# Kernel optimization log

Measured on AMD Instinct MI355X. Metric: run time of the kernel, lower is better.

## Reference

```python
import jax, jax.numpy as jnp
import numpy as np

BUCKET_SIZE = 64
N_HASHES = 8
SELF_ATTN_VALUE = -5e4  # TOKEN_SELF_ATTN_VALUE
EPS = 1e-12  # F.normalize eps


def setup_inputs() -> dict:
    key = jax.random.key(0)
    k1, k2, k3 = jax.random.split(key, 3)
    B, S, D = 16, 4096, 128
    n_buckets = S // BUCKET_SIZE  # 64
    qk = jax.random.normal(k1, (B, S, D), dtype=jnp.float32)
    v = jax.random.normal(k2, (B, S, D), dtype=jnp.float32)
    # rotations_shape = (1, dim, n_hashes, n_buckets // 2); shared across batch
    rotations = jax.random.normal(k3, (1, D, N_HASHES, n_buckets // 2), dtype=jnp.float32)
    return {"qk": qk, "v": v, "rotations": rotations}


def _hash_vectors(qk, rotations, n_buckets):
    # qk: (B,S,D), rotations: (1,D,H,n_buckets//2)
    rotated = jnp.einsum('btf,fhi->bhti', qk, rotations[0])  # (B,H,S,nb/2)
    rotated = jnp.concatenate([rotated, -rotated], axis=-1)   # (B,H,S,nb)
    buckets = jnp.argmax(rotated, axis=-1)                    # (B,H,S)
    offsets = (jnp.arange(N_HASHES) * n_buckets)[None, :, None]
    return (buckets + offsets).reshape(qk.shape[0], -1)       # (B, H*S)


def _look_one_back(x):
    # concat each chunk with its predecessor (circular), along the window dim
    return jnp.concatenate([x, jnp.roll(x, 1, axis=1)], axis=2)


def reference(qk, v, rotations):
    B, S, D = qk.shape
    H = N_HASHES
    n_buckets = S // BUCKET_SIZE
    buckets = _hash_vectors(qk, rotations, n_buckets)         # (B, H*S) int

    ticker = jnp.broadcast_to(jnp.arange(H * S)[None, :], (B, H * S))
    buckets_and_t = S * buckets + (ticker % S)                # unique keys
    sticker = jnp.argsort(buckets_and_t, axis=-1)             # sort by bucket
    undo_sort = jnp.argsort(sticker, axis=-1)

    st = sticker % S                                          # original positions
    sqk = jnp.take_along_axis(qk, st[..., None], axis=1)      # (B,H*S,D)
    sv = jnp.take_along_axis(v, st[..., None], axis=1)

    C = H * n_buckets                                         # num chunks
    bq_t = st.reshape(B, C, -1)                               # (B,C,w)
    bqk = sqk.reshape(B, C, -1, D)
    bv = sv.reshape(B, C, -1, D)
    bq = bqk
    nrm = jnp.maximum(jnp.linalg.norm(bqk, axis=-1, keepdims=True), EPS)
    bk = bqk / nrm                                            # F.normalize

    bk = _look_one_back(bk)                                   # (B,C,2w,D)
    bv = _look_one_back(bv)
    bkv_t = _look_one_back(bq_t)                              # (B,C,2w)

    dots = jnp.einsum('bcie,bcje->bcij', bq, bk) * (D ** -0.5)  # (B,C,w,2w)
    self_mask = bq_t[:, :, :, None] == bkv_t[:, :, None, :]
    dots = jnp.where(self_mask, SELF_ATTN_VALUE, dots)

    lse = jax.scipy.special.logsumexp(dots, axis=-1, keepdims=True)
    probs = jnp.exp(dots - lse)
    bo = jnp.einsum('bcij,bcje->bcie', probs, bv)             # (B,C,w,D)

    so = bo.reshape(B, -1, D)                                 # (B,H*S,D)
    slogits = lse.reshape(B, -1)                              # (B,H*S)
    o = jnp.take_along_axis(so, undo_sort[..., None], axis=1)
    logits = jnp.take_along_axis(slogits, undo_sort, axis=1)

    o = o.reshape(B, H, S, D)
    logits = logits.reshape(B, H, S, 1)
    w = jnp.exp(logits - jax.scipy.special.logsumexp(logits, axis=1, keepdims=True))
    out = jnp.sum(o * w, axis=1)                              # (B,S,D)
    return out
```

## Files before the change

kernel.cpp:

```cpp
#include <hip/hip_runtime.h>
#include <hip/hip_bf16.h>


#define B_ 16
#define S_ 4096
#define D_ 128
#define H_ 8
#define C_ 512
#define SCALE_ 0.08838834764831845f

typedef __attribute__((ext_vector_type(8))) short bf16x8;
typedef __attribute__((ext_vector_type(8))) _Float16 f16x8;
typedef __attribute__((ext_vector_type(2))) _Float16 f16x2t;
typedef __attribute__((ext_vector_type(4))) float f32x4;
typedef __attribute__((ext_vector_type(2))) float f32x2v;
typedef __attribute__((ext_vector_type(4))) int int4v;

union BF8U { int4v i; bf16x8 b; };
union F16x8U { int4v i; f16x8 h; };

__device__ __forceinline__ unsigned hi_pack(float x0, float x1) {
    unsigned a, b;
    __builtin_memcpy(&b, &x0, 4);
    __builtin_memcpy(&a, &x1, 4);
    return __builtin_amdgcn_perm(a, b, 0x07060302u);
}
__device__ __forceinline__ float truncbf(float x) {
    unsigned u; __builtin_memcpy(&u, &x, 4);
    u &= 0xFFFF0000u;
    float f; __builtin_memcpy(&f, &u, 4);
    return f;
}
__device__ __forceinline__ unsigned pack2f16(float x0, float x1) {
    f16x2t h = {(_Float16)x0, (_Float16)x1};
    unsigned u; __builtin_memcpy(&u, &h, 4);
    return u;
}
__device__ __forceinline__ unsigned enc_ks(unsigned u) {
    return (u & 0x80000000u) ? ~u : (u | 0x80000000u);
}
__device__ __forceinline__ float dec_ks(unsigned ks) {
    unsigned u = (ks & 0x80000000u) ? (ks ^ 0x80000000u) : ~ks;
    float f; __builtin_memcpy(&f, &u, 4);
    return f;
}

__global__ __launch_bounds__(256) void norm_kernel(const float* __restrict__ qk,
                                                   float* __restrict__ rnrm) {
    int half = threadIdx.x >> 5;
    int lane32 = threadIdx.x & 31;
    size_t row = (size_t)blockIdx.x * 8 + half;
    float4 vv = ((const float4*)(qk + row * D_))[lane32];
    float ss = vv.x * vv.x + vv.y * vv.y + vv.z * vv.z + vv.w * vv.w;
    #pragma unroll
    for (int m = 1; m < 32; m <<= 1) ss += __shfl_xor(ss, m, 64);
    if (lane32 == 0) rnrm[row] = 1.0f / fmaxf(sqrtf(ss), 1e-12f);
}

__global__ __launch_bounds__(256) void prep_rot_kernel(const float* __restrict__ rot,
                                                       short* __restrict__ rth,
                                                       short* __restrict__ rtl) {
    int x = blockIdx.x * 256 + threadIdx.x;
    int hp = x >> 11;
    int ia = (x >> 5) & 63;
    int ft = x & 31;
    float v0 = rot[(size_t)(ft * 4 + 0) * 256 + hp * 64 + ia];
    float v1 = rot[(size_t)(ft * 4 + 1) * 256 + hp * 64 + ia];
    float v2 = rot[(size_t)(ft * 4 + 2) * 256 + hp * 64 + ia];
    float v3 = rot[(size_t)(ft * 4 + 3) * 256 + hp * 64 + ia];
    unsigned h0 = hi_pack(v0, v1), h1 = hi_pack(v2, v3);
    unsigned l0 = hi_pack(v0 - truncbf(v0), v1 - truncbf(v1));
    unsigned l1 = hi_pack(v2 - truncbf(v2), v3 - truncbf(v3));
    int off = ia * 128 + ((((ft >> 1) ^ (ia & 7)) << 3) | ((ft & 1) << 2));
    *(int2*)&rth[hp * 8192 + off] = make_int2((int)h0, (int)h1);
    *(int2*)&rtl[hp * 8192 + off] = make_int2((int)l0, (int)l1);
}

__global__ __launch_bounds__(256, 4) void hash_kernel(
        const float* __restrict__ qk, const float* __restrict__ rot,
        const short* __restrict__ rth, const short* __restrict__ rtl,
        int* __restrict__ buckets) {
    __shared__ unsigned char flags[2][64];

    const int bid = blockIdx.x;
    const int b = bid >> 8;
    const int tile = (bid >> 2) & 63;
    const int hp = bid & 3;
    const int tid = threadIdx.x;
    const int w = tid >> 6, l = tid & 63, g = l >> 4, m = l & 15;

    if (tid < 8) ((int4*)flags)[tid] = make_int4(0, 0, 0, 0);
    __syncthreads();

    const float* qrow = qk + ((size_t)b * S_ + (size_t)tile * 64 + w * 16 + m) * D_;
    bf16x8 qh[4], qlr[4];
    #pragma unroll
    for (int s = 0; s < 4; ++s) {
        float4 xa = *(const float4*)(qrow + s * 32 + g * 8);
        float4 xb = *(const float4*)(qrow + s * 32 + g * 8 + 4);
        BF8U hu, lu;
        hu.i[0] = (int)hi_pack(xa.x, xa.y); hu.i[1] = (int)hi_pack(xa.z, xa.w);
        hu.i[2] = (int)hi_pack(xb.x, xb.y); hu.i[3] = (int)hi_pack(xb.z, xb.w);
        lu.i[0] = (int)hi_pack(xa.x - truncbf(xa.x), xa.y - truncbf(xa.y));
        lu.i[1] = (int)hi_pack(xa.z - truncbf(xa.z), xa.w - truncbf(xa.w));
        lu.i[2] = (int)hi_pack(xb.x - truncbf(xb.x), xb.y - truncbf(xb.y));
        lu.i[3] = (int)hi_pack(xb.z - truncbf(xb.z), xb.w - truncbf(xb.w));
        qh[s] = hu.b; qlr[s] = lu.b;
    }

    f32x4 dots_n[4];
    #pragma unroll
    for (int nt = 0; nt < 4; ++nt) {
        f32x4 acc = (f32x4){0.f, 0.f, 0.f, 0.f};
        #pragma unroll
        for (int s = 0; s < 4; ++s) {
            int kr = hp * 8192 + (nt * 16 + m) * 128 + (((s * 4 + g) ^ (m & 7)) << 3);
            bf16x8 bh = *(const bf16x8*)&rth[kr];
            bf16x8 bl = *(const bf16x8*)&rtl[kr];
            acc = __builtin_amdgcn_mfma_f32_16x16x32_bf16(qh[s], bh, acc, 0, 0, 0);
            acc = __builtin_amdgcn_mfma_f32_16x16x32_bf16(qh[s], bl, acc, 0, 0, 0);
            acc = __builtin_amdgcn_mfma_f32_16x16x32_bf16(qlr[s], bh, acc, 0, 0, 0);
        }
        dots_n[nt] = acc;
    }

    #pragma unroll
    for (int hh = 0; hh < 2; ++hh) {
        int h = hp * 2 + hh;
        #pragma unroll
        for (int r = 0; r < 4; ++r) {
            unsigned long long kM = 0ull, kS = 0ull;
            #pragma unroll
            for (int nn = 0; nn < 2; ++nn) {
                float v = dots_n[hh * 2 + nn][r];
                unsigned u; __builtin_memcpy(&u, &v, 4);
                int i = nn * 16 + m;
                unsigned long long kp =
                    ((unsigned long long)enc_ks(u) << 6) | (unsigned)(63 - i);
                unsigned long long kn =
                    ((unsigned long long)enc_ks(u ^ 0x80000000u) << 6) |
                    (unsigned)(63 - (i + 32));
                if (kp > kM) { kS = kM; kM = kp; } else if (kp > kS) kS = kp;
                if (kn > kM) { kS = kM; kM = kn; } else if (kn > kS) kS = kn;
            }
            #pragma unroll
            for (int st = 1; st <= 8; st <<= 1) {
                unsigned long long oM = __shfl_xor(kM, st, 64);
                unsigned long long oS = __shfl_xor(kS, st, 64);
                unsigned long long lo = kM < oM ? kM : oM;
                kM = kM > oM ? kM : oM;
                unsigned long long hs = kS > oS ? kS : oS;
                kS = hs > lo ? hs : lo;
            }
            if (m == 0) {
                int tok = w * 16 + g * 4 + r;
                int i1 = 63 - (int)(kM & 63ull);
                float v1 = dec_ks((unsigned)(kM >> 6));
                float v2 = dec_ks((unsigned)(kS >> 6));
                if (v1 - v2 < 2e-2f) flags[hh][tok] = 1;
                buckets[(((size_t)(b * H_ + h)) << 12) + tile * 64 + tok] = i1;
            }
        }
    }
    __syncthreads();

    int tok = tid >> 2, part = tid & 3;
    const float* qtok = qk + ((size_t)b * S_ + (size_t)tile * 64 + tok) * D_;
    for (int hh = 0; hh < 2; ++hh) {
        if (!flags[hh][tok]) continue;
        int h = hp * 2 + hh;
        double pd[8] = {0, 0, 0, 0, 0, 0, 0, 0};
        #pragma unroll 2
        for (int f = 0; f < 128; ++f) {
            double q = (double)qtok[f];
            const float* rp = rot + (size_t)f * 256 + h * 32 + part * 8;
            float4 r0 = *(const float4*)rp;
            float4 r1 = *(const float4*)(rp + 4);
            pd[0] = fma(q, (double)r0.x, pd[0]);
            pd[1] = fma(q, (double)r0.y, pd[1]);
            pd[2] = fma(q, (double)r0.z, pd[2]);
            pd[3] = fma(q, (double)r0.w, pd[3]);
            pd[4] = fma(q, (double)r1.x, pd[4]);
            pd[5] = fma(q, (double)r1.y, pd[5]);
            pd[6] = fma(q, (double)r1.z, pd[6]);
            pd[7] = fma(q, (double)r1.w, pd[7]);
        }
        double bv = -1e300; int bi = 0;
        #pragma unroll
        for (int ii = 0; ii < 8; ++ii) {
            int i = part * 8 + ii;
            double v = pd[ii];
            if (v > bv || (v == bv && i < bi)) { bv = v; bi = i; }
            double nv = -v; int ni = i + 32;
            if (nv > bv || (nv == bv && ni < bi)) { bv = nv; bi = ni; }
        }
        #pragma unroll
        for (int mm = 1; mm <= 2; mm <<= 1) {
            double ov = __shfl_xor(bv, mm, 64);
            int oi = __shfl_xor(bi, mm, 64);
            if (ov > bv || (ov == bv && oi < bi)) { bv = ov; bi = oi; }
        }
        if (part == 0)
            buckets[(((size_t)(b * H_ + h)) << 12) + tile * 64 + tok] = bi;
    }
}

__global__ __launch_bounds__(256) void sort_kernel(const int* __restrict__ buckets,
                                                   int* __restrict__ st,
                                                   int* __restrict__ inv,
                                                   const float* __restrict__ rnrm,
                                                   float* __restrict__ rnrm_s) {
    __shared__ unsigned short hist[256][64];
    __shared__ int base[64];
    __shared__ int totals[64];
    int tid = threadIdx.x;
    const int* bkrow = buckets + (size_t)blockIdx.x * S_;
    const float* rnb = rnrm + (size_t)(blockIdx.x >> 3) * S_;

    unsigned int* h32 = (unsigned int*)hist;
    #pragma unroll
    for (int u = 0; u < 32; ++u) h32[u * 256 + tid] = 0;
    __syncthreads();

    #pragma unroll
    for (int u = 0; u < 16; ++u) {
        int t = tid * 16 + u;
        int bk = bkrow[t];
        hist[tid][bk]++;
    }
    __syncthreads();

    if (tid < 64) {
        int bucket = tid;
        int run = 0;
        for (int ch = 0; ch < 256; ++ch) {
            int v = hist[ch][bucket];
            hist[ch][bucket] = (unsigned short)run;
            run += v;
        }
        totals[bucket] = run;
    }
    __syncthreads();
    if (tid == 0) {
        int acc = 0;
        for (int k = 0; k < 64; ++k) { base[k] = acc; acc += totals[k]; }
    }
    __syncthreads();

    int* strow = st + (size_t)blockIdx.x * S_;
    int* invrow = inv + (size_t)blockIdx.x * S_;
    float* rnsrow = rnrm_s + (size_t)blockIdx.x * S_;
    #pragma unroll
    for (int u = 0; u < 16; ++u) {
        int t = tid * 16 + u;
        int bk = bkrow[t];
        int off = hist[tid][bk];
        hist[tid][bk] = (unsigned short)(off + 1);
        int pos = base[bk] + off;
        strow[pos] = t;
        invrow[t] = pos;
        rnsrow[pos] = rnb[t] * SCALE_;
    }
}

__device__ __forceinline__ void transpose4(const float4 v, int g, float (&w_)[4]) {
    bool b0 = (g & 1) != 0, b1 = (g & 2) != 0;
    float k0 = b1 ? v.z : v.x;
    float k1 = b1 ? v.w : v.y;
    float s0 = b1 ? v.x : v.z;
    float s1 = b1 ? v.y : v.w;
    float r0 = __shfl_xor(s0, 32, 64);
    float r1 = __shfl_xor(s1, 32, 64);
    float kq_ = b0 ? k1 : k0;
    float rq_ = b0 ? r1 : r0;
    float sk  = b0 ? k0 : k1;
    float sr  = b0 ? r0 : r1;
    float tk_ = __shfl_xor(sk, 16, 64);
    float tr_ = __shfl_xor(sr, 16, 64);
    float A0 = b0 ? tk_ : kq_;
    float A1 = b0 ? kq_ : tk_;
    float B0 = b0 ? tr_ : rq_;
    float B1 = b0 ? rq_ : tr_;
    w_[0] = b1 ? B0 : A0;
    w_[1] = b1 ? B1 : A1;
    w_[2] = b1 ? A0 : B0;
    w_[3] = b1 ? A1 : B1;
}

template<bool DENSE>
__global__ __launch_bounds__(256, 4) void attn_mfma_kernel(
        const float* __restrict__ qk, const float* __restrict__ rnrm_s,
        const float* __restrict__ vglob, const int* __restrict__ st,
        float* __restrict__ outnum, float* __restrict__ den,
        _Float16* __restrict__ snum, float* __restrict__ sden) {
    __shared__ int tq_s[64];
    __shared__ int tk1_s[64];
    __shared__ float rns0[64];
    __shared__ float rns1[64];
    __shared__ short kbuf[8192];
    __shared__ short vbuf[8192];

    const int p = blockIdx.x;
    const int bc = (p & 7) * 1024 + (p >> 3);
    const int b  = bc >> 9;
    const int c  = bc & 511;
    const int tid = threadIdx.x;
    const int w   = tid >> 6;
    const int l   = tid & 63;
    const int g   = l >> 4;
    const int m   = l & 15;
    const size_t bS = ((size_t)b << 12);
    const int* stb = st + ((size_t)b << 15);

    const int c1 = (c + 511) & 511;
    if (tid < 64) {
        tq_s[tid]  = stb[c * 64 + tid];
        tk1_s[tid] = stb[c1 * 64 + tid];
        rns0[tid] = rnrm_s[(((size_t)(b * H_ + (c >> 6))) << 12) + (size_t)(c & 63) * 64 + tid];
        rns1[tid] = rnrm_s[(((size_t)(b * H_ + (c1 >> 6))) << 12) + (size_t)(c1 & 63) * 64 + tid];
    }
    __syncthreads();

    const int qtok_m = tq_s[w * 16 + m];

    f16x8 qh[4];
    f32x4 e4[4];
    f32x4 acc_o[8];
    #pragma unroll
    for (int dt = 0; dt < 8; ++dt) acc_o[dt] = (f32x4){0.f, 0.f, 0.f, 0.f};
    float densum = 0.0f;

    float4 kreg[8];
    float4 va[4], vb[4];

    auto issue_k = [&](const int* __restrict__ toks) {
        #pragma unroll
        for (int u = 0; u < 8; ++u) {
            int token = u * 8 + (tid >> 5);
            int cc = tid & 31;
            kreg[u] = *(const float4*)(qk + (bS + toks[token]) * D_ + cc * 4);
        }
    };
    auto write_k = [&]() {
        #pragma unroll
        for (int u = 0; u < 8; ++u) {
            int token = u * 8 + (tid >> 5);
            int cc = tid & 31;
            float4 vv = kreg[u];
            unsigned h0 = pack2f16(vv.x, vv.y), h1 = pack2f16(vv.z, vv.w);
            int kw = token * 128 + ((((cc >> 1) ^ (token & 7)) << 3) | ((cc & 1) << 2));
            *(int2*)&kbuf[kw] = make_int2((int)h0, (int)h1);
        }
    };
    auto issue_v = [&](const int* __restrict__ toks) {
        #pragma unroll
        for (int up = 0; up < 4; ++up) {
            int kq8 = w * 16 + (up & 1) * 8;
            int cc = (up >> 1) * 16 + m;
            va[up] = *(const float4*)(vglob + (bS + toks[kq8 + g]) * D_ + cc * 4);
            vb[up] = *(const float4*)(vglob + (bS + toks[kq8 + 4 + g]) * D_ + cc * 4);
        }
    };
    auto write_v = [&]() {
        #pragma unroll
        for (int up = 0; up < 4; ++up) {
            int kq8 = w * 16 + (up & 1) * 8;
            int cc = (up >> 1) * 16 + m;
            float wa[4], wb[4];
            transpose4(va[up], g, wa);
            transpose4(vb[up], g, wb);
            unsigned h0 = pack2f16(wa[0], wa[1]), h1 = pack2f16(wa[2], wa[3]);
            unsigned h2 = pack2f16(wb[0], wb[1]), h3 = pack2f16(wb[2], wb[3]);
            int d = cc * 4 + g;
            int ds = d ^ ((d >> 3) & 7);
            int kg = kq8 >> 3;
            int idx = (kg * 128 + ds) * 8;
            *(int4*)&vbuf[idx] = make_int4((int)h0, (int)h1, (int)h2, (int)h3);
        }
    };
    auto qk_pass = [&](int mode, const float* __restrict__ rns,
                       const int* __restrict__ tkp) {
        #pragma unroll
        for (int kt = 0; kt < 4; ++kt) {
            f32x4 acc = (f32x4){0.f, 0.f, 0.f, 0.f};
            #pragma unroll
            for (int s4 = 0; s4 < 4; ++s4) {
                int kr = (kt * 16 + m) * 128 + (((s4 * 4 + g) ^ (m & 7)) << 3);
                f16x8 ah = *(const f16x8*)&kbuf[kr];
                acc = __builtin_amdgcn_mfma_f32_16x16x32_f16(ah, qh[s4], acc, 0, 0, 0);
            }
            f32x4 rn4 = *(const f32x4*)&rns[kt * 16 + g * 4];
            int4v kt4;
            if (mode == 1) kt4 = *(const int4v*)&tkp[kt * 16 + g * 4];
            f32x4 e;
            #pragma unroll
            for (int r = 0; r < 4; ++r) {
                float ev = __expf(acc[r] * rn4[r]);
                if (mode == 0) {
                    if (kt == w && (g * 4 + r) == m) ev = 0.0f;
                } else {
                    if (kt4[r] == qtok_m) ev = 0.0f;
                }
                e[r] = ev;
                densum += ev;
            }
            e4[kt] = e;
        }
    };
    auto pv_pass = [&]() {
        #pragma unroll
        for (int s = 0; s < 2; ++s) {
            float pav[8];
            #pragma unroll
            for (int c2 = 0; c2 < 2; ++c2) {
                int srcLane = ((g & 1) * 2 + c2) * 16 + m;
                #pragma unroll
                for (int r = 0; r < 4; ++r) {
                    float v0 = __shfl(e4[2 * s][r], srcLane, 64);
                    float v1 = __shfl(e4[2 * s + 1][r], srcLane, 64);
                    pav[c2 * 4 + r] = (g >> 1) ? v1 : v0;
                }
            }
            F16x8U pahu;
            #pragma unroll
            for (int j2 = 0; j2 < 4; ++j2)
                pahu.i[j2] = (int)pack2f16(pav[2 * j2], pav[2 * j2 + 1]);
            f16x8 pah = pahu.h;
            #pragma unroll
            for (int dt = 0; dt < 8; ++dt) {
                int d = dt * 16 + m;
                int ds = d ^ ((d >> 3) & 7);
                int base = ((s * 4 + g) * 128 + ds) * 8;
                f16x8 vh = *(const f16x8*)&vbuf[base];
                acc_o[dt] = __builtin_amdgcn_mfma_f32_16x16x32_f16(pah, vh, acc_o[dt], 0, 0, 0);
            }
        }
    };

    issue_k(tq_s);
    write_k();
    __syncthreads();

    #pragma unroll
    for (int s4 = 0; s4 < 4; ++s4) {
        int qr = (w * 16 + m) * 128 + (((s4 * 4 + g) ^ (m & 7)) << 3);
        qh[s4] = *(const f16x8*)&kbuf[qr];
    }
    issue_v(tq_s);
    qk_pass(0, rns0, tq_s);
    write_v();
    __syncthreads();

    issue_k(tk1_s);
    pv_pass();
    write_k();
    __syncthreads();

    issue_v(tk1_s);
    qk_pass(1, rns1, tk1_s);
    write_v();
    __syncthreads();

    pv_pass();

    densum += __shfl_xor(densum, 16, 64);
    densum += __shfl_xor(densum, 32, 64);

    if (DENSE) {
        const int h = c >> 6;
        const size_t base = (((size_t)(b * H_ + h)) << 12) + (size_t)(c & 63) * 64;
        #pragma unroll
        for (int r = 0; r < 4; ++r) {
            int row = w * 16 + g * 4 + r;
            _Float16* nrow = snum + (base + row) * D_;
            #pragma unroll
            for (int dt = 0; dt < 8; ++dt)
                __builtin_nontemporal_store((_Float16)acc_o[dt][r], nrow + dt * 16 + m);
        }
        if (g == 0) __builtin_nontemporal_store(densum, sden + base + w * 16 + m);
    } else {
        if (g == 0) atomicAdd(den + bS + qtok_m, densum);
        int4v q4tok = *(const int4v*)&tq_s[w * 16 + g * 4];
        #pragma unroll
        for (int r = 0; r < 4; ++r) {
            float* obase = outnum + ((bS + q4tok[r]) * D_);
            #pragma unroll
            for (int dt = 0; dt < 8; ++dt)
                atomicAdd(obase + dt * 16 + m, acc_o[dt][r]);
        }
    }
}

__global__ __launch_bounds__(256) void combine_kernel(
        const _Float16* __restrict__ snum, const float* __restrict__ sden,
        const int* __restrict__ inv, float* __restrict__ out) {
    int wv = threadIdx.x >> 6, l = threadIdx.x & 63;
    int t = blockIdx.x * 4 + wv;
    int b = t >> 12, s = t & 4095;
    float s0 = 0.f, s1 = 0.f, dsum = 0.f;
    #pragma unroll
    for (int h = 0; h < H_; ++h) {
        int bh = b * H_ + h;
        int pos = inv[((size_t)bh << 12) + s];
        size_t row = ((size_t)bh << 12) + pos;
        dsum += __builtin_nontemporal_load(sden + row);
        unsigned uv = __builtin_nontemporal_load(
            (const unsigned*)(snum + row * D_ + 2 * l));
        unsigned short us0 = (unsigned short)(uv & 0xFFFFu);
        unsigned short us1 = (unsigned short)(uv >> 16);
        _Float16 h0, h1;
        __builtin_memcpy(&h0, &us0, 2);
        __builtin_memcpy(&h1, &us1, 2);
        s0 += (float)h0;
        s1 += (float)h1;
    }
    float rd = 1.0f / dsum;
    f32x2v o2 = {s0 * rd, s1 * rd};
    __builtin_nontemporal_store(o2, (f32x2v*)(out + (size_t)t * D_ + 2 * l));
}

__global__ __launch_bounds__(256) void div_kernel(float* __restrict__ out,
                                                  const float* __restrict__ den) {
    int i = blockIdx.x * 256 + threadIdx.x;
    float4 o = ((float4*)out)[i];
    float dn = den[i >> 5];
    ((float4*)out)[i] = make_float4(o.x / dn, o.y / dn, o.z / dn, o.w / dn);
}

extern "C" void kernel_launch(void* const* d_in, const int* in_sizes, int n_in,
                              void* d_out, int out_size, void* d_ws, size_t ws_size,
                              hipStream_t stream) {
    const float* qk  = (const float*)d_in[0];
    const float* v   = (const float*)d_in[1];
    const float* rot = (const float*)d_in[2];
    float* out = (float*)d_out;

    char* ws = (char*)d_ws;
    float* rnrm    = (float*)ws;
    int* buckets   = (int*)(ws + 262144);
    int* inv       = buckets;
    int* st        = (int*)(ws + 2359296);
    float* rnrm_s  = (float*)(ws + 4456448);
    float* sden    = (float*)(ws + 6553600);
    short* rth     = (short*)(ws + 8650752);
    short* rtl     = (short*)(ws + 8716288);
    _Float16* snum = (_Float16*)(ws + 8781824);
    const size_t need = 8781824ull + 134217728ull;

    norm_kernel<<<B_ * S_ / 8, 256, 0, stream>>>(qk, rnrm);
    prep_rot_kernel<<<32, 256, 0, stream>>>(rot, rth, rtl);
    hash_kernel<<<B_ * (S_ / 64) * 4, 256, 0, stream>>>(qk, rot, rth, rtl, buckets);
    sort_kernel<<<B_ * H_, 256, 0, stream>>>(buckets, st, inv, rnrm, rnrm_s);

    if (ws_size >= need) {
        attn_mfma_kernel<true><<<B_ * C_, 256, 0, stream>>>(
            qk, rnrm_s, v, st, nullptr, nullptr, snum, sden);
        combine_kernel<<<B_ * S_ / 4, 256, 0, stream>>>(snum, sden, inv, out);
    } else {
        float* den = sden;
        hipMemsetAsync(out, 0, (size_t)B_ * S_ * D_ * 4, stream);
        hipMemsetAsync(den, 0, (size_t)B_ * S_ * 4, stream);
        attn_mfma_kernel<false><<<B_ * C_, 256, 0, stream>>>(
            qk, rnrm_s, v, st, out, den, nullptr, nullptr);
        div_kernel<<<B_ * S_ * D_ / 4 / 256, 256, 0, stream>>>(out, den);
    }
}
```

Before: 263.1 us.

## Pre-convert qk and v to fp16 once so attention gathers half the bytes

The norm kernel becomes a convert kernel that also writes fp16 copies of qk and v into workspace. The attention kernel then gathers fp16 rows instead of fp32 rows and converts nothing on the fly. Each token is gathered about 16 times across hashes and look-back, so halving the gathered bytes should cut memory traffic. The cost is an extra pass that writes 32 MB, plus a larger workspace requirement, which could push execution onto the fallback path if the workspace is too small.

```diff
diff --git a/kernel.cpp b/kernel.cpp
--- a/kernel.cpp
+++ b/kernel.cpp
@@ -36,6 +36,12 @@
     unsigned u; __builtin_memcpy(&u, &h, 4);
     return u;
 }
+__device__ __forceinline__ unsigned lo_pair(unsigned t0, unsigned t1) {
+    return __builtin_amdgcn_perm(t1, t0, 0x05040100u);
+}
+__device__ __forceinline__ unsigned hi_pair(unsigned t0, unsigned t1) {
+    return __builtin_amdgcn_perm(t1, t0, 0x07060302u);
+}
 __device__ __forceinline__ unsigned enc_ks(unsigned u) {
     return (u & 0x80000000u) ? ~u : (u | 0x80000000u);
 }
@@ -45,16 +51,27 @@
     return f;
 }
 
-__global__ __launch_bounds__(256) void norm_kernel(const float* __restrict__ qk,
-                                                   float* __restrict__ rnrm) {
+__global__ __launch_bounds__(256) void cvt_kernel(const float* __restrict__ qk,
+                                                  const float* __restrict__ v,
+                                                  _Float16* __restrict__ qkh,
+                                                  _Float16* __restrict__ vh,
+                                                  float* __restrict__ rnrm) {
+    int nb = (int)gridDim.x >> 1;
+    bool isV = (int)blockIdx.x >= nb;
+    const float* src = isV ? v : qk;
+    _Float16* dst = isV ? vh : qkh;
     int half = threadIdx.x >> 5;
     int lane32 = threadIdx.x & 31;
-    size_t row = (size_t)blockIdx.x * 8 + half;
-    float4 vv = ((const float4*)(qk + row * D_))[lane32];
-    float ss = vv.x * vv.x + vv.y * vv.y + vv.z * vv.z + vv.w * vv.w;
-    #pragma unroll
-    for (int m = 1; m < 32; m <<= 1) ss += __shfl_xor(ss, m, 64);
-    if (lane32 == 0) rnrm[row] = 1.0f / fmaxf(sqrtf(ss), 1e-12f);
+    size_t row = (size_t)((int)blockIdx.x - (isV ? nb : 0)) * 8 + half;
+    float4 vv = ((const float4*)(src + row * D_))[lane32];
+    if (!isV) {
+        float ss = vv.x * vv.x + vv.y * vv.y + vv.z * vv.z + vv.w * vv.w;
+        #pragma unroll
+        for (int m = 1; m < 32; m <<= 1) ss += __shfl_xor(ss, m, 64);
+        if (lane32 == 0) rnrm[row] = 1.0f / fmaxf(sqrtf(ss), 1e-12f);
+    }
+    unsigned u0 = pack2f16(vv.x, vv.y), u1 = pack2f16(vv.z, vv.w);
+    *(int2*)(dst + row * D_ + lane32 * 4) = make_int2((int)u0, (int)u1);
 }
 
 __global__ __launch_bounds__(256) void prep_rot_kernel(const float* __restrict__ rot,
@@ -289,8 +306,8 @@
 
 template<bool DENSE>
 __global__ __launch_bounds__(256, 4) void attn_mfma_kernel(
-        const float* __restrict__ qk, const float* __restrict__ rnrm_s,
-        const float* __restrict__ vglob, const int* __restrict__ st,
+        const _Float16* __restrict__ qkh, const float* __restrict__ rnrm_s,
+        const _Float16* __restrict__ vh, const int* __restrict__ st,
         float* __restrict__ outnum, float* __restrict__ den,
         _Float16* __restrict__ snum, float* __restrict__ sden) {
     __shared__ int tq_s[64];
@@ -330,52 +347,57 @@
     for (int dt = 0; dt < 8; ++dt) acc_o[dt] = (f32x4){0.f, 0.f, 0.f, 0.f};
     float densum = 0.0f;
 
-    float4 kreg[8];
-    float4 va[4], vb[4];
+    int4 kreg4[4];
+    int4 va16[2], vb16[2];
 
     auto issue_k = [&](const int* __restrict__ toks) {
         #pragma unroll
-        for (int u = 0; u < 8; ++u) {
-            int token = u * 8 + (tid >> 5);
-            int cc = tid & 31;
-            kreg[u] = *(const float4*)(qk + (bS + toks[token]) * D_ + cc * 4);
+        for (int u = 0; u < 4; ++u) {
+            int fi = u * 256 + tid;
+            int token = fi >> 4, cc = fi & 15;
+            kreg4[u] = *(const int4*)(qkh + (bS + toks[token]) * D_ + cc * 8);
         }
     };
     auto write_k = [&]() {
         #pragma unroll
-        for (int u = 0; u < 8; ++u) {
-            int token = u * 8 + (tid >> 5);
-            int cc = tid & 31;
-            float4 vv = kreg[u];
-            unsigned h0 = pack2f16(vv.x, vv.y), h1 = pack2f16(vv.z, vv.w);
-            int kw = token * 128 + ((((cc >> 1) ^ (token & 7)) << 3) | ((cc & 1) << 2));
-            *(int2*)&kbuf[kw] = make_int2((int)h0, (int)h1);
+        for (int u = 0; u < 4; ++u) {
+            int fi = u * 256 + tid;
+            int token = fi >> 4, cc = fi & 15;
+            int kw = token * 128 + ((cc ^ (token & 7)) << 3);
+            *(int4*)&kbuf[kw] = kreg4[u];
         }
     };
     auto issue_v = [&](const int* __restrict__ toks) {
         #pragma unroll
-        for (int up = 0; up < 4; ++up) {
-            int kq8 = w * 16 + (up & 1) * 8;
-            int cc = (up >> 1) * 16 + m;
-            va[up] = *(const float4*)(vglob + (bS + toks[kq8 + g]) * D_ + cc * 4);
-            vb[up] = *(const float4*)(vglob + (bS + toks[kq8 + 4 + g]) * D_ + cc * 4);
+        for (int up = 0; up < 2; ++up) {
+            int kg = w * 2 + up;
+            va16[up] = *(const int4*)(vh + (bS + toks[kg * 8 + g]) * D_ + m * 8);
+            vb16[up] = *(const int4*)(vh + (bS + toks[kg * 8 + 4 + g]) * D_ + m * 8);
         }
     };
     auto write_v = [&]() {
         #pragma unroll
-        for (int up = 0; up < 4; ++up) {
-            int kq8 = w * 16 + (up & 1) * 8;
-            int cc = (up >> 1) * 16 + m;
+        for (int up = 0; up < 2; ++up) {
+            int kg = w * 2 + up;
             float wa[4], wb[4];
-            transpose4(va[up], g, wa);
-            transpose4(vb[up], g, wb);
-            unsigned h0 = pack2f16(wa[0], wa[1]), h1 = pack2f16(wa[2], wa[3]);
-            unsigned h2 = pack2f16(wb[0], wb[1]), h3 = pack2f16(wb[2], wb[3]);
-            int d = cc * 4 + g;
-            int ds = d ^ ((d >> 3) & 7);
-            int kg = kq8 >> 3;
-            int idx = (kg * 128 + ds) * 8;
-            *(int4*)&vbuf[idx] = make_int4((int)h0, (int)h1, (int)h2, (int)h3);
+            float4 vaf, vbf;
+            __builtin_memcpy(&vaf, &va16[up], 16);
+            __builtin_memcpy(&vbf, &vb16[up], 16);
+            transpose4(vaf, g, wa);
+            transpose4(vbf, g, wb);
+            unsigned ua[4], ub[4];
+            __builtin_memcpy(ua, wa, 16);
+            __builtin_memcpy(ub, wb, 16);
+            int d0 = 8 * m + 2 * g;
+            int ds0 = d0 ^ ((d0 >> 3) & 7);
+            int d1 = d0 + 1;
+            int ds1 = d1 ^ ((d1 >> 3) & 7);
+            int4 rowlo = make_int4((int)lo_pair(ua[0], ua[1]), (int)lo_pair(ua[2], ua[3]),
+                                   (int)lo_pair(ub[0], ub[1]), (int)lo_pair(ub[2], ub[3]));
+            int4 rowhi = make_int4((int)hi_pair(ua[0], ua[1]), (int)hi_pair(ua[2], ua[3]),
+                                   (int)hi_pair(ub[0], ub[1]), (int)hi_pair(ub[2], ub[3]));
+            *(int4*)&vbuf[(kg * 128 + ds0) * 8] = rowlo;
+            *(int4*)&vbuf[(kg * 128 + ds1) * 8] = rowhi;
         }
     };
     auto qk_pass = [&](int mode, const float* __restrict__ rns,
@@ -431,8 +453,8 @@
                 int d = dt * 16 + m;
                 int ds = d ^ ((d >> 3) & 7);
                 int base = ((s * 4 + g) * 128 + ds) * 8;
-                f16x8 vh = *(const f16x8*)&vbuf[base];
-                acc_o[dt] = __builtin_amdgcn_mfma_f32_16x16x32_f16(pah, vh, acc_o[dt], 0, 0, 0);
+                f16x8 vhf = *(const f16x8*)&vbuf[base];
+                acc_o[dt] = __builtin_amdgcn_mfma_f32_16x16x32_f16(pah, vhf, acc_o[dt], 0, 0, 0);
             }
         }
     };
@@ -544,24 +566,26 @@
     float* sden    = (float*)(ws + 6553600);
     short* rth     = (short*)(ws + 8650752);
     short* rtl     = (short*)(ws + 8716288);
-    _Float16* snum = (_Float16*)(ws + 8781824);
-    const size_t need = 8781824ull + 134217728ull;
-
-    norm_kernel<<<B_ * S_ / 8, 256, 0, stream>>>(qk, rnrm);
+    _Float16* qkh  = (_Float16*)(ws + 8781824);
+    _Float16* vh   = (_Float16*)(ws + 25559040);
+    _Float16* snum = (_Float16*)(ws + 42336256);
+    const size_t need = 42336256ull + 134217728ull;
+
+    cvt_kernel<<<B_ * S_ / 4, 256, 0, stream>>>(qk, v, qkh, vh, rnrm);
     prep_rot_kernel<<<32, 256, 0, stream>>>(rot, rth, rtl);
     hash_kernel<<<B_ * (S_ / 64) * 4, 256, 0, stream>>>(qk, rot, rth, rtl, buckets);
     sort_kernel<<<B_ * H_, 256, 0, stream>>>(buckets, st, inv, rnrm, rnrm_s);
 
     if (ws_size >= need) {
         attn_mfma_kernel<true><<<B_ * C_, 256, 0, stream>>>(
-            qk, rnrm_s, v, st, nullptr, nullptr, snum, sden);
+            qkh, rnrm_s, vh, st, nullptr, nullptr, snum, sden);
         combine_kernel<<<B_ * S_ / 4, 256, 0, stream>>>(snum, sden, inv, out);
     } else {
         float* den = sden;
         hipMemsetAsync(out, 0, (size_t)B_ * S_ * D_ * 4, stream);
         hipMemsetAsync(den, 0, (size_t)B_ * S_ * 4, stream);
         attn_mfma_kernel<false><<<B_ * C_, 256, 0, stream>>>(
-            qk, rnrm_s, v, st, out, den, nullptr, nullptr);
+            qkh, rnrm_s, vh, st, out, den, nullptr, nullptr);
         div_kernel<<<B_ * S_ * D_ / 4 / 256, 256, 0, stream>>>(out, den);
     }
 }
```

Result: slower. 275.0 us (+4.5%).
